# Optimization experiments

Hardware: AMD Instinct MI355X
Metric: run time of the kernel (lower is better)

Reference implementation:

```python
import jax, jax.numpy as jnp
import numpy as np

N = 100000
E = 1600000
IN_C, HID, NCLS = 128, 64, 40


def setup_inputs() -> dict:
    key = jax.random.key(0)
    k1, k2, k3, k4 = jax.random.split(key, 4)
    x = jax.random.normal(k1, (N, IN_C), dtype=jnp.float32)
    edge_index = jax.random.randint(k2, (2, E), 0, N, dtype=jnp.int64)
    # Glorot-ish init for the two GCNConv layers
    W1 = jax.random.normal(k3, (IN_C, HID), dtype=jnp.float32) / np.sqrt(IN_C)
    b1 = jnp.zeros((HID,), dtype=jnp.float32)
    W2 = jax.random.normal(k4, (HID, NCLS), dtype=jnp.float32) / np.sqrt(HID)
    b2 = jnp.zeros((NCLS,), dtype=jnp.float32)
    return {"x": x, "edge_index": edge_index, "W1": W1, "b1": b1, "W2": W2, "b2": b2}


def _gcn_norm(edge_index, n):
    # add self-loops, compute symmetric normalization (PyG gcn_norm defaults)
    loops = jnp.arange(n, dtype=edge_index.dtype)
    src = jnp.concatenate([edge_index[0], loops])
    dst = jnp.concatenate([edge_index[1], loops])
    deg = jax.ops.segment_sum(jnp.ones_like(dst, dtype=jnp.float32), dst, num_segments=n)
    dis = jnp.where(deg > 0, jax.lax.rsqrt(jnp.maximum(deg, 1.0)), 0.0)
    norm = dis[src] * dis[dst]  # [E+N]
    return src, dst, norm


def _gcn_conv(x, W, b, src, dst, norm, n):
    h = x @ W                      # [N, out]
    msg = h[src] * norm[:, None]   # gather + scale, [E+N, out]
    out = jax.ops.segment_sum(msg, dst, num_segments=n)  # scatter-add
    return out + b


def reference(x, edge_index, W1, b1, W2, b2):
    n = x.shape[0]
    src, dst, norm = _gcn_norm(edge_index, n)
    h = jax.nn.relu(_gcn_conv(x, W1, b1, src, dst, norm, n))
    return _gcn_conv(h, W2, b2, src, dst, norm, n)
```

## Files before the change

kernel.cpp:

```cpp
#include <hip/hip_runtime.h>

#define IN_C 128
#define HID  64
#define NCLS 40
#define CHP  2048
#define SPT  512
#define CHH  4096
#define NB   1024

typedef float f32x4 __attribute__((ext_vector_type(4)));
typedef short s16x8 __attribute__((ext_vector_type(8)));

static __device__ inline unsigned short f2bf(float f) {
    unsigned u = __float_as_uint(f);
    return (unsigned short)((u + 0x7FFF + ((u >> 16) & 1)) >> 16);
}

static __device__ inline void split1(float v, unsigned short& hb, unsigned short& lb) {
    hb = (unsigned short)(__float_as_uint(v) >> 16);
    float vhi = __uint_as_float((unsigned)hb << 16);
    lb = (unsigned short)(__float_as_uint(v - vhi) >> 16);
}

static __device__ inline void split8(const f32x4 a0, const f32x4 a1, s16x8& hi, s16x8& lo) {
    float v[8] = {a0.x, a0.y, a0.z, a0.w, a1.x, a1.y, a1.z, a1.w};
#pragma unroll
    for (int j = 0; j < 8; ++j) {
        unsigned short hb, lb;
        split1(v[j], hb, lb);
        hi[j] = (short)hb;
        lo[j] = (short)lb;
    }
}


__global__ __launch_bounds__(256) void bhist_kernel(
    const int* __restrict__ dst, int* __restrict__ bcnt, int E, int B)
{
    __shared__ int h[NB];
    const int t = threadIdx.x;
    for (int i = t; i < NB; i += 256) h[i] = 0;
    __syncthreads();
    const int base = blockIdx.x * CHH;
    const int nE = min(CHH, E - base);
    for (int k = t; k < nE; k += 256) atomicAdd(&h[dst[base + k] >> 7], 1);
    __syncthreads();
    for (int b = t; b < B; b += 256) { int c = h[b]; if (c) atomicAdd(&bcnt[b], c); }
}


__global__ __launch_bounds__(256) void bscan_kernel(
    const int* __restrict__ bcnt, int* __restrict__ bptr, int* __restrict__ bfill,
    int B, int E)
{
    __shared__ int s[256];
    const int t = threadIdx.x;
    int v[4]; int ts = 0;
#pragma unroll
    for (int j = 0; j < 4; ++j) {
        int idx = 4 * t + j;
        v[j] = (idx < B) ? bcnt[idx] : 0;
        ts += v[j];
    }
    s[t] = ts; __syncthreads();
    for (int off = 1; off < 256; off <<= 1) {
        int add = (t >= off) ? s[t - off] : 0;
        __syncthreads();
        s[t] += add;
        __syncthreads();
    }
    int run = s[t] - ts;
#pragma unroll
    for (int j = 0; j < 4; ++j) {
        int idx = 4 * t + j;
        if (idx < B) { bptr[idx] = run; bfill[idx] = run; run += v[j]; }
    }
    if (t == 0) bptr[B] = E;
}


__global__ __launch_bounds__(SPT) void scatter_part(
    const int* __restrict__ src, const int* __restrict__ dst,
    int* __restrict__ bfill, int* __restrict__ part, int E, int B)
{
    __shared__ int cnt[NB], soff[NB], gpos[NB], sdata[SPT];
    __shared__ int stage[CHP], destg[CHP];
    const int t = threadIdx.x;
    const int base = blockIdx.x * CHP;
    const int nE = min(CHP, E - base);

    for (int i = t; i < NB; i += SPT) cnt[i] = 0;
    __syncthreads();
    for (int k = t; k < nE; k += SPT)
        atomicAdd(&cnt[dst[base + k] >> 7], 1);
    __syncthreads();
    int v0 = cnt[2 * t], v1 = cnt[2 * t + 1];
    int ts = v0 + v1;
    sdata[t] = ts; __syncthreads();
    for (int off = 1; off < SPT; off <<= 1) {
        int add = (t >= off) ? sdata[t - off] : 0;
        __syncthreads();
        sdata[t] += add;
        __syncthreads();
    }
    int run = sdata[t] - ts;
    soff[2 * t] = run;
    soff[2 * t + 1] = run + v0;
    __syncthreads();
    for (int b = t; b < B; b += SPT) {
        int c = cnt[b];
        gpos[b] = c ? atomicAdd(&bfill[b], c) : 0;
    }
    __syncthreads();
    for (int i = t; i < NB; i += SPT) cnt[i] = 0;
    __syncthreads();
    for (int k = t; k < nE; k += SPT) {
        int d = dst[base + k];
        int b = d >> 7;
        int p = atomicAdd(&cnt[b], 1);
        int o = soff[b] + p;
        stage[o] = (src[base + k] << 7) | (d & 127);
        destg[o] = gpos[b] + p;
    }
    __syncthreads();
    for (int k = t; k < nE; k += SPT)
        part[destg[k]] = stage[k];
}


__global__ __launch_bounds__(256) void fine_sort(
    const int* __restrict__ bptr, const int* __restrict__ part,
    int* __restrict__ col, int* __restrict__ ptr, float* __restrict__ dis,
    int n, int E)
{
    __shared__ int cnt[128], sc[128], cur[128];
    __shared__ int stage[3072];
    const int t = threadIdx.x;
    const int base = blockIdx.x << 7;
    const int nn = min(128, n - base);
    const int rstart = bptr[blockIdx.x];
    const int rend   = bptr[blockIdx.x + 1];

    if (t < 128) cnt[t] = 0;
    __syncthreads();
    for (int e = rstart + t; e < rend; e += 256)
        atomicAdd(&cnt[part[e] & 127], 1);
    __syncthreads();
    int v = (t < 128) ? cnt[t] : 0;
    if (t < 128) sc[t] = v;
    __syncthreads();
    for (int off = 1; off < 128; off <<= 1) {
        int add = (t < 128 && t >= off) ? sc[t - off] : 0;
        __syncthreads();
        if (t < 128) sc[t] += add;
        __syncthreads();
    }
    if (t < 128) cur[t] = sc[t] - v;
    if (t < nn) {
        ptr[base + t] = rstart + sc[t] - v;
        dis[base + t] = rsqrtf((float)(v + 1));
    }
    if (blockIdx.x == 0 && t == 0) ptr[n] = E;
    __syncthreads();
    for (int e = rstart + t; e < rend; e += 256) {
        int pk = part[e];
        int p = atomicAdd(&cur[pk & 127], 1);
        int s = pk >> 7;
        if (p < 3072) stage[p] = s;
        else col[rstart + p] = s;
    }
    __syncthreads();
    int sz = rend - rstart; if (sz > 3072) sz = 3072;
    for (int j = t; j < sz; j += 256) col[rstart + j] = stage[j];
}


__global__ __launch_bounds__(256) void gemm1_mfma(
    const float* __restrict__ x, const float* __restrict__ W1,
    const float* __restrict__ dis, unsigned short* __restrict__ hs1b, int n)
{
    const int wave = threadIdx.x >> 6;
    const int lane = threadIdx.x & 63;
    const int m    = lane & 15;
    const int q    = lane >> 4;
    const int col  = wave * 16 + m;

    s16x8 bhi[4], blo[4];
#pragma unroll
    for (int t = 0; t < 4; ++t) {
#pragma unroll
        for (int j = 0; j < 8; ++j) {
            int k = t * 32 + q * 8 + j;
            unsigned short hb, lb;
            split1(W1[k * HID + col], hb, lb);
            bhi[t][j] = (short)hb;
            blo[t][j] = (short)lb;
        }
    }

    const int nslab = n >> 4;
    for (int s = blockIdx.x; s < nslab; s += gridDim.x) {
        const float* xrow = x + (size_t)(s * 16 + m) * IN_C;
        f32x4 acc = {0.f, 0.f, 0.f, 0.f};
#pragma unroll
        for (int t = 0; t < 4; ++t) {
            f32x4 a0 = *(const f32x4*)(xrow + t * 32 + q * 8);
            f32x4 a1 = *(const f32x4*)(xrow + t * 32 + q * 8 + 4);
            s16x8 ahi, alo;
            split8(a0, a1, ahi, alo);
            acc = __builtin_amdgcn_mfma_f32_16x16x32_bf16(ahi, bhi[t], acc, 0, 0, 0);
            acc = __builtin_amdgcn_mfma_f32_16x16x32_bf16(alo, bhi[t], acc, 0, 0, 0);
            acc = __builtin_amdgcn_mfma_f32_16x16x32_bf16(ahi, blo[t], acc, 0, 0, 0);
        }
#pragma unroll
        for (int r = 0; r < 4; ++r) {
            int row = s * 16 + q * 4 + r;
            hs1b[(size_t)row * HID + col] = f2bf(acc[r] * dis[row]);
        }
    }
}


__global__ __launch_bounds__(256) void agg1_kernel(
    const int* __restrict__ ptr, const int* __restrict__ col,
    const unsigned* __restrict__ hs1p, const float* __restrict__ dis,
    const float* __restrict__ b1, unsigned* __restrict__ h1p, int n)
{
    int wave = threadIdx.x >> 6, lane = threadIdx.x & 63;
    int i = blockIdx.x * 4 + wave;
    if (i >= n) return;
    const int h  = lane >> 5;
    const int hl = lane & 31;
    const int ZR = n;
    int start = ptr[i], end = ptr[i + 1];
    unsigned sw = hs1p[(unsigned)i * 32u + (unsigned)hl];
    float dd = dis[i];
    float acc0 = 0.f, acc1 = 0.f;
    for (int base = start; base < end; base += 64) {
        int m = end - base; if (m > 64) m = 64;
        int myc = (lane < m) ? col[base + lane] : ZR;
        int rounds = (m + 1) >> 1;
        for (int j = 0; j < rounds; j += 8) {
            unsigned w[8];
#pragma unroll
            for (int u = 0; u < 8; ++u) {
                int s = __shfl(myc, 2 * (j + u) + h);
                w[u] = hs1p[(unsigned)s * 32u + (unsigned)hl];
            }
#pragma unroll
            for (int u = 0; u < 8; ++u) {
                acc0 += __uint_as_float(w[u] << 16);
                acc1 += __uint_as_float(w[u] & 0xffff0000u);
            }
        }
    }
    float o0 = acc0 + __shfl(acc0, (lane + 32) & 63);
    float o1 = acc1 + __shfl(acc1, (lane + 32) & 63);
    if (lane < 32) {
        float2 bb = *(const float2*)&b1[2 * lane];
        float v0 = (o0 + __uint_as_float(sw << 16)) * dd + bb.x;
        float v1 = (o1 + __uint_as_float(sw & 0xffff0000u)) * dd + bb.y;
        v0 = v0 > 0.f ? v0 : 0.f;
        v1 = v1 > 0.f ? v1 : 0.f;
        h1p[(unsigned)i * 32u + (unsigned)lane] = (unsigned)f2bf(v0) | ((unsigned)f2bf(v1) << 16);
    }
}


__global__ __launch_bounds__(192) void gemm2_mfma(
    const unsigned short* __restrict__ h1b, const float* __restrict__ W2,
    const float* __restrict__ dis, unsigned short* __restrict__ hs2b, int n)
{
    const int wave = threadIdx.x >> 6;
    const int lane = threadIdx.x & 63;
    const int m    = lane & 15;
    const int q    = lane >> 4;
    const int col  = wave * 16 + m;

    s16x8 bhi[2], blo[2];
#pragma unroll
    for (int t = 0; t < 2; ++t) {
#pragma unroll
        for (int j = 0; j < 8; ++j) {
            int k = t * 32 + q * 8 + j;
            float w = (col < NCLS) ? W2[k * NCLS + col] : 0.f;
            unsigned short hb, lb;
            split1(w, hb, lb);
            bhi[t][j] = (short)hb;
            blo[t][j] = (short)lb;
        }
    }

    const int nslab = n >> 4;
    for (int s = blockIdx.x; s < nslab; s += gridDim.x) {
        const unsigned short* hrow = h1b + (size_t)(s * 16 + m) * HID;
        f32x4 acc = {0.f, 0.f, 0.f, 0.f};
#pragma unroll
        for (int t = 0; t < 2; ++t) {
            s16x8 ahi = *(const s16x8*)(hrow + t * 32 + q * 8);
            acc = __builtin_amdgcn_mfma_f32_16x16x32_bf16(ahi, bhi[t], acc, 0, 0, 0);
            acc = __builtin_amdgcn_mfma_f32_16x16x32_bf16(ahi, blo[t], acc, 0, 0, 0);
        }
        if (col < NCLS) {
#pragma unroll
            for (int r = 0; r < 4; ++r) {
                int row = s * 16 + q * 4 + r;
                hs2b[(size_t)row * NCLS + col] = f2bf(acc[r] * dis[row]);
            }
        }
    }
}


__global__ __launch_bounds__(256) void agg2_kernel(
    const int* __restrict__ ptr, const int* __restrict__ col,
    const unsigned* __restrict__ hs2p, const float* __restrict__ dis,
    const float* __restrict__ b2, float* __restrict__ out, int n)
{
    int wave = threadIdx.x >> 6, lane = threadIdx.x & 63;
    int i = blockIdx.x * 4 + wave;
    if (i >= n) return;
    const int g  = lane / 20;
    const int gl = lane - g * 20;
    const bool act = g < 3;
    int start = ptr[i], end = ptr[i + 1];
    unsigned sw = hs2p[(unsigned)i * 20u + (unsigned)gl];
    float dd = dis[i];
    float acc0 = 0.f, acc1 = 0.f;
    for (int base = start; base < end; base += 64) {
        int m = end - base; if (m > 64) m = 64;
        int myc = (lane < m) ? col[base + lane] : 0;
        int j = 0;
        for (; 24 * (j / 8 + 1) <= m; j += 8) {
            unsigned w[8];
#pragma unroll
            for (int u = 0; u < 8; ++u) {
                int s = __shfl(myc, 3 * (j + u) + g);
                w[u] = hs2p[(unsigned)s * 20u + (unsigned)gl];
            }
#pragma unroll
            for (int u = 0; u < 8; ++u) {
                acc0 += __uint_as_float(w[u] << 16);
                acc1 += __uint_as_float(w[u] & 0xffff0000u);
            }
        }
        int rounds = (m + 2) / 3;
        for (; j < rounds; j += 8) {
            unsigned w[8]; int ok[8];
#pragma unroll
            for (int u = 0; u < 8; ++u) {
                int e = 3 * (j + u) + g;
                ok[u] = act && (e < m);
                int s = __shfl(myc, ok[u] ? e : 0);
                w[u] = hs2p[(unsigned)s * 20u + (unsigned)gl];
            }
#pragma unroll
            for (int u = 0; u < 8; ++u) {
                acc0 += ok[u] ? __uint_as_float(w[u] << 16) : 0.f;
                acc1 += ok[u] ? __uint_as_float(w[u] & 0xffff0000u) : 0.f;
            }
        }
    }
    float t0 = acc0 + __shfl(acc0, (lane + 20) & 63) + __shfl(acc0, (lane + 40) & 63);
    float t1 = acc1 + __shfl(acc1, (lane + 20) & 63) + __shfl(acc1, (lane + 40) & 63);
    float2 bb = *(const float2*)&b2[2 * gl];
    float v0 = (t0 + __uint_as_float(sw << 16)) * dd + bb.x;
    float v1 = (t1 + __uint_as_float(sw & 0xffff0000u)) * dd + bb.y;
    float a = __shfl(v0, lane >> 1);
    float b = __shfl(v1, lane >> 1);
    if (lane < NCLS) out[(size_t)i * NCLS + lane] = (lane & 1) ? b : a;
}


extern "C" void kernel_launch(void* const* d_in, const int* in_sizes, int n_in,
                              void* d_out, int out_size, void* d_ws, size_t ws_size,
                              hipStream_t stream) {
    const float* x  = (const float*)d_in[0];
    const int*   ei = (const int*)d_in[1];
    const float* W1 = (const float*)d_in[2];
    const float* b1 = (const float*)d_in[3];
    const float* W2 = (const float*)d_in[4];
    const float* b2 = (const float*)d_in[5];
    float* out = (float*)d_out;

    const int n = in_sizes[0] / IN_C;
    const int E = in_sizes[1] / 2;
    const int B = (n + 127) >> 7;
    const int* src = ei;
    const int* dst = ei + E;

    char* ws = (char*)d_ws;
    size_t off = 0;
    auto alloc = [&](size_t bytes) { char* p = ws + off; off += (bytes + 255) & ~(size_t)255; return p; };
    float* dis  = (float*)alloc((size_t)n * 4);
    int*   ptr  = (int*)  alloc((size_t)(n + 1) * 4);
    int*   col  = (int*)  alloc((size_t)E * 4);
    int*   bcnt = (int*)  alloc((size_t)NB * 4);
    int*   bptr = (int*)  alloc((size_t)(NB + 1) * 4);
    int*   bfill= (int*)  alloc((size_t)NB * 4);
    unsigned short* hs1b = (unsigned short*)alloc((size_t)(n + 1) * HID * 2);
    unsigned short* h1b  = (unsigned short*)alloc((size_t)n * HID * 2);
    unsigned short* hs2b = (unsigned short*)alloc((size_t)(n + 1) * NCLS * 2);
    int* part = (int*)alloc((size_t)E * 4);

    hipMemsetAsync(bcnt, 0, (size_t)B * 4, stream);
    hipMemsetAsync(hs1b + (size_t)n * HID, 0, HID * 2, stream);
    bhist_kernel<<<(E + CHH - 1) / CHH, 256, 0, stream>>>(dst, bcnt, E, B);
    bscan_kernel<<<1, 256, 0, stream>>>(bcnt, bptr, bfill, B, E);
    scatter_part<<<(E + CHP - 1) / CHP, SPT, 0, stream>>>(src, dst, bfill, part, E, B);
    fine_sort<<<B, 256, 0, stream>>>(bptr, part, col, ptr, dis, n, E);

    gemm1_mfma<<<2048, 256, 0, stream>>>(x, W1, dis, hs1b, n);
    agg1_kernel<<<(n + 3) / 4, 256, 0, stream>>>(ptr, col, (const unsigned*)hs1b, dis, b1,
                                                 (unsigned*)h1b, n);
    gemm2_mfma<<<2048, 192, 0, stream>>>(h1b, W2, dis, hs2b, n);
    agg2_kernel<<<(n + 3) / 4, 256, 0, stream>>>(ptr, col, (const unsigned*)hs2b, dis, b2,
                                                 out, n);
}
```

Before: 258.4 us.

## Replace two-level bucket sort CSR build with global atomic counting sort

Drops the coarse bucket histogram, partition scatter and per-bucket fine sort, and builds the CSR with three kernels instead: a per-node global atomic degree histogram, a single-block scan over all nodes that also writes dis, and a per-edge atomic scatter into col. This removes the intermediate part buffer and the shared-memory staging passes. In exchange it relies on many global atomics to random addresses and a serial scan of about 100 per thread in one block. The order of neighbours within each row becomes nondeterministic, which changes the floating-point summation order.

```diff
diff --git a/kernel.cpp b/kernel.cpp
--- a/kernel.cpp
+++ b/kernel.cpp
@@ -3,10 +3,7 @@
 #define IN_C 128
 #define HID  64
 #define NCLS 40
-#define CHP  2048
-#define SPT  512
-#define CHH  4096
-#define NB   1024
+#define SCT  512
 
 typedef float f32x4 __attribute__((ext_vector_type(4)));
 typedef short s16x8 __attribute__((ext_vector_type(8)));
@@ -34,144 +31,64 @@
 }
 
 
-__global__ __launch_bounds__(256) void bhist_kernel(
-    const int* __restrict__ dst, int* __restrict__ bcnt, int E, int B)
-{
-    __shared__ int h[NB];
+__global__ __launch_bounds__(SCT) void deg_hist(
+    const int* __restrict__ dst, int* __restrict__ deg, int E)
+{
+    int k = blockIdx.x * SCT + threadIdx.x;
+    if (k < E) atomicAdd(&deg[dst[k]], 1);
+}
+
+
+__global__ __launch_bounds__(1024) void scan_deg(
+    const int* __restrict__ deg, int* __restrict__ ptr, int* __restrict__ pfill,
+    float* __restrict__ dis, int n, int E)
+{
+    __shared__ int sums[1024];
     const int t = threadIdx.x;
-    for (int i = t; i < NB; i += 256) h[i] = 0;
+    const int chunk = (((n + 1023) >> 10) + 3) & ~3;
+    const int lo = t * chunk;
+    const int hi = min(n, lo + chunk);
+
+    int ts = 0;
+    if (lo < n) {
+        int nv = (hi - lo) >> 2;
+        const int4* dv = (const int4*)(deg + lo);
+        for (int j = 0; j < nv; ++j) {
+            int4 v = dv[j];
+            ts += v.x + v.y + v.z + v.w;
+        }
+        for (int i = lo + (nv << 2); i < hi; ++i) ts += deg[i];
+    }
+    sums[t] = ts;
     __syncthreads();
-    const int base = blockIdx.x * CHH;
-    const int nE = min(CHH, E - base);
-    for (int k = t; k < nE; k += 256) atomicAdd(&h[dst[base + k] >> 7], 1);
-    __syncthreads();
-    for (int b = t; b < B; b += 256) { int c = h[b]; if (c) atomicAdd(&bcnt[b], c); }
-}
-
-
-__global__ __launch_bounds__(256) void bscan_kernel(
-    const int* __restrict__ bcnt, int* __restrict__ bptr, int* __restrict__ bfill,
-    int B, int E)
-{
-    __shared__ int s[256];
-    const int t = threadIdx.x;
-    int v[4]; int ts = 0;
-#pragma unroll
-    for (int j = 0; j < 4; ++j) {
-        int idx = 4 * t + j;
-        v[j] = (idx < B) ? bcnt[idx] : 0;
-        ts += v[j];
-    }
-    s[t] = ts; __syncthreads();
-    for (int off = 1; off < 256; off <<= 1) {
-        int add = (t >= off) ? s[t - off] : 0;
+    for (int off = 1; off < 1024; off <<= 1) {
+        int add = (t >= off) ? sums[t - off] : 0;
         __syncthreads();
-        s[t] += add;
+        sums[t] += add;
         __syncthreads();
     }
-    int run = s[t] - ts;
-#pragma unroll
-    for (int j = 0; j < 4; ++j) {
-        int idx = 4 * t + j;
-        if (idx < B) { bptr[idx] = run; bfill[idx] = run; run += v[j]; }
-    }
-    if (t == 0) bptr[B] = E;
-}
-
-
-__global__ __launch_bounds__(SPT) void scatter_part(
+    int run = sums[t] - ts;
+
+    for (int i = lo; i < hi; ++i) {
+        int d = deg[i];
+        ptr[i] = run;
+        pfill[i] = run;
+        dis[i] = rsqrtf((float)(d + 1));
+        run += d;
+    }
+    if (t == 0) ptr[n] = E;
+}
+
+
+__global__ __launch_bounds__(SCT) void scatter_col(
     const int* __restrict__ src, const int* __restrict__ dst,
-    int* __restrict__ bfill, int* __restrict__ part, int E, int B)
-{
-    __shared__ int cnt[NB], soff[NB], gpos[NB], sdata[SPT];
-    __shared__ int stage[CHP], destg[CHP];
-    const int t = threadIdx.x;
-    const int base = blockIdx.x * CHP;
-    const int nE = min(CHP, E - base);
-
-    for (int i = t; i < NB; i += SPT) cnt[i] = 0;
-    __syncthreads();
-    for (int k = t; k < nE; k += SPT)
-        atomicAdd(&cnt[dst[base + k] >> 7], 1);
-    __syncthreads();
-    int v0 = cnt[2 * t], v1 = cnt[2 * t + 1];
-    int ts = v0 + v1;
-    sdata[t] = ts; __syncthreads();
-    for (int off = 1; off < SPT; off <<= 1) {
-        int add = (t >= off) ? sdata[t - off] : 0;
-        __syncthreads();
-        sdata[t] += add;
-        __syncthreads();
-    }
-    int run = sdata[t] - ts;
-    soff[2 * t] = run;
-    soff[2 * t + 1] = run + v0;
-    __syncthreads();
-    for (int b = t; b < B; b += SPT) {
-        int c = cnt[b];
-        gpos[b] = c ? atomicAdd(&bfill[b], c) : 0;
-    }
-    __syncthreads();
-    for (int i = t; i < NB; i += SPT) cnt[i] = 0;
-    __syncthreads();
-    for (int k = t; k < nE; k += SPT) {
-        int d = dst[base + k];
-        int b = d >> 7;
-        int p = atomicAdd(&cnt[b], 1);
-        int o = soff[b] + p;
-        stage[o] = (src[base + k] << 7) | (d & 127);
-        destg[o] = gpos[b] + p;
-    }
-    __syncthreads();
-    for (int k = t; k < nE; k += SPT)
-        part[destg[k]] = stage[k];
-}
-
-
-__global__ __launch_bounds__(256) void fine_sort(
-    const int* __restrict__ bptr, const int* __restrict__ part,
-    int* __restrict__ col, int* __restrict__ ptr, float* __restrict__ dis,
-    int n, int E)
-{
-    __shared__ int cnt[128], sc[128], cur[128];
-    __shared__ int stage[3072];
-    const int t = threadIdx.x;
-    const int base = blockIdx.x << 7;
-    const int nn = min(128, n - base);
-    const int rstart = bptr[blockIdx.x];
-    const int rend   = bptr[blockIdx.x + 1];
-
-    if (t < 128) cnt[t] = 0;
-    __syncthreads();
-    for (int e = rstart + t; e < rend; e += 256)
-        atomicAdd(&cnt[part[e] & 127], 1);
-    __syncthreads();
-    int v = (t < 128) ? cnt[t] : 0;
-    if (t < 128) sc[t] = v;
-    __syncthreads();
-    for (int off = 1; off < 128; off <<= 1) {
-        int add = (t < 128 && t >= off) ? sc[t - off] : 0;
-        __syncthreads();
-        if (t < 128) sc[t] += add;
-        __syncthreads();
-    }
-    if (t < 128) cur[t] = sc[t] - v;
-    if (t < nn) {
-        ptr[base + t] = rstart + sc[t] - v;
-        dis[base + t] = rsqrtf((float)(v + 1));
-    }
-    if (blockIdx.x == 0 && t == 0) ptr[n] = E;
-    __syncthreads();
-    for (int e = rstart + t; e < rend; e += 256) {
-        int pk = part[e];
-        int p = atomicAdd(&cur[pk & 127], 1);
-        int s = pk >> 7;
-        if (p < 3072) stage[p] = s;
-        else col[rstart + p] = s;
-    }
-    __syncthreads();
-    int sz = rend - rstart; if (sz > 3072) sz = 3072;
-    for (int j = t; j < sz; j += 256) col[rstart + j] = stage[j];
+    int* __restrict__ pfill, int* __restrict__ col, int E)
+{
+    int k = blockIdx.x * SCT + threadIdx.x;
+    if (k >= E) return;
+    int d = dst[k];
+    int p = atomicAdd(&pfill[d], 1);
+    if ((unsigned)p < (unsigned)E) col[p] = src[k];
 }
 
 
@@ -385,30 +302,27 @@
 
     const int n = in_sizes[0] / IN_C;
     const int E = in_sizes[1] / 2;
-    const int B = (n + 127) >> 7;
     const int* src = ei;
     const int* dst = ei + E;
 
     char* ws = (char*)d_ws;
     size_t off = 0;
     auto alloc = [&](size_t bytes) { char* p = ws + off; off += (bytes + 255) & ~(size_t)255; return p; };
-    float* dis  = (float*)alloc((size_t)n * 4);
-    int*   ptr  = (int*)  alloc((size_t)(n + 1) * 4);
-    int*   col  = (int*)  alloc((size_t)E * 4);
-    int*   bcnt = (int*)  alloc((size_t)NB * 4);
-    int*   bptr = (int*)  alloc((size_t)(NB + 1) * 4);
-    int*   bfill= (int*)  alloc((size_t)NB * 4);
+    float* dis   = (float*)alloc((size_t)n * 4);
+    int*   ptr   = (int*)  alloc((size_t)(n + 1) * 4);
+    int*   pfill = (int*)  alloc((size_t)n * 4);
+    int*   col   = (int*)  alloc((size_t)E * 4);
+    int*   deg   = (int*)  alloc((size_t)n * 4);
     unsigned short* hs1b = (unsigned short*)alloc((size_t)(n + 1) * HID * 2);
     unsigned short* h1b  = (unsigned short*)alloc((size_t)n * HID * 2);
     unsigned short* hs2b = (unsigned short*)alloc((size_t)(n + 1) * NCLS * 2);
-    int* part = (int*)alloc((size_t)E * 4);
-
-    hipMemsetAsync(bcnt, 0, (size_t)B * 4, stream);
+
+    hipMemsetAsync(deg, 0, (size_t)n * 4, stream);
     hipMemsetAsync(hs1b + (size_t)n * HID, 0, HID * 2, stream);
-    bhist_kernel<<<(E + CHH - 1) / CHH, 256, 0, stream>>>(dst, bcnt, E, B);
-    bscan_kernel<<<1, 256, 0, stream>>>(bcnt, bptr, bfill, B, E);
-    scatter_part<<<(E + CHP - 1) / CHP, SPT, 0, stream>>>(src, dst, bfill, part, E, B);
-    fine_sort<<<B, 256, 0, stream>>>(bptr, part, col, ptr, dis, n, E);
+
+    deg_hist<<<(E + SCT - 1) / SCT, SCT, 0, stream>>>(dst, deg, E);
+    scan_deg<<<1, 1024, 0, stream>>>(deg, ptr, pfill, dis, n, E);
+    scatter_col<<<(E + SCT - 1) / SCT, SCT, 0, stream>>>(src, dst, pfill, col, E);
 
     gemm1_mfma<<<2048, 256, 0, stream>>>(x, W1, dis, hs1b, n);
     agg1_kernel<<<(n + 3) / 4, 256, 0, stream>>>(ptr, col, (const unsigned*)hs1b, dis, b1,
```

Result: slower. 643.2 us (+148.9%).
